# Kernel tuning notes

Measured on AMD Instinct MI355X. Metric: run time of the kernel, lower is better.

## Reference

```python
import jax, jax.numpy as jnp
import numpy as np

WAY = 5  # N_way from init


def setup_inputs() -> dict:
    key = jax.random.key(0)
    k1, k2, k3, k4 = jax.random.split(key, 4)
    N, c, h, w = 80, 2048, 16, 16
    S = 512  # shuffle_num
    x = jax.random.normal(k1, (N, c, h, w), dtype=jnp.float32)
    s_ca = jax.random.uniform(k2, (N, c, 1, 1), dtype=jnp.float32)
    # random channel indices per sample (stand-in for random.sample)
    rand_index = jax.random.randint(k3, (N, S), 0, c)
    # partner offset per sample (stand-in for random j != i)
    partner = jax.random.randint(k4, (N,), 0, N - 1)
    return {"x": x, "s_ca": s_ca, "rand_index": rand_index,
            "partner": partner, "shuffle_num": S}


def reference(x, s_ca, rand_index, partner, shuffle_num):
    N, c, h, w = x.shape
    way = WAY
    scores = s_ca.reshape(N, c)
    # per-sample top-k channels by attention score
    _, topk_idx = jax.lax.top_k(scores, shuffle_num)          # [N, S]
    # partner sample j != i (offset trick guarantees inequality)
    j = (jnp.arange(N) + 1 + partner) % N                      # [N]
    bi = jnp.arange(N)[:, None]                                # [N, 1]
    x_topk = x[bi, topk_idx]                                   # [N, S, h, w]
    x_part = x[j[:, None], rand_index]                         # [N, S, h, w]
    blend = 0.7 * x_topk + 0.3 * x_part
    # scatter blended channels back (batched gather-blend-scatter)
    aug_x = x.at[bi, topk_idx].set(blend)                      # [N, c, h, w]
    # group into (way, shot, ...) and concat original + augmented episodes
    x_r = x.reshape(way, -1, c, h, w)
    aug_r = aug_x.reshape(way, -1, c, h, w)
    out = jnp.concatenate((x_r, aug_r), axis=1)                # [way, 2*shot, c, h, w]
    s = s_ca.reshape(way, -1, c, 1, 1)
    s = jnp.concatenate((s, s), axis=1)                        # repeat(1,2,1,1,1)
    out = out * s
    return out.reshape(-1, c, h, w)                            # [2N, c, h, w]
```

## Files before the change

kernel.cpp:

```cpp
#include <hip/hip_runtime.h>

#define N_SAMP 80
#define C_CH   2048
#define HW     256
#define S_TOP  512
#define HW4    64

__global__ __launch_bounds__(256) void rank_lds_kernel(
    const float* __restrict__ s_ca, int* __restrict__ rank) {
  __shared__ unsigned long long keys[C_CH];
  const int n = blockIdx.x >> 3;
  const int tid = threadIdx.x;
  const float* __restrict__ row = s_ca + (size_t)n * C_CH;

  for (int i = tid; i < C_CH; i += 256) {
    unsigned int b = __float_as_uint(row[i]);
    b ^= (b & 0x80000000u) ? 0xFFFFFFFFu : 0x80000000u;
    keys[i] = ((unsigned long long)b << 11) |
              (unsigned long long)(C_CH - 1 - i);
  }
  __syncthreads();

  const int i = ((blockIdx.x & 7) << 8) | tid;
  const unsigned long long ki = keys[i];
  int cnt = 0;
#pragma unroll 16
  for (int j = 0; j < C_CH; ++j) {
    cnt += (keys[j] > ki) ? 1 : 0;
  }
  rank[(size_t)n * C_CH + i] = (cnt < S_TOP) ? cnt : -1;
}

__global__ __launch_bounds__(256) void shuffle_out_fused(
    const float4* __restrict__ x4, const float* __restrict__ s_ca,
    const int* __restrict__ rand_index, const int* __restrict__ partner,
    const int* __restrict__ rank, float4* __restrict__ out4) {
  const unsigned int lane = threadIdx.x & 63u;
  const unsigned int pw = blockIdx.x * 4u + (threadIdx.x >> 6);
  const unsigned int n = pw >> 11;
  const unsigned int ch = pw & 2047u;
  const unsigned int g = n >> 4;
  const unsigned int b = n & 15u;

  const size_t out_plain =
      (((size_t)((g << 5) | b) * C_CH + ch) << 6) | lane;
  const size_t out_aug = out_plain + ((size_t)(16 * C_CH) << 6);

  const float s = s_ca[pw];
  const float4 v = x4[((size_t)pw << 6) | lane];
  float4 pv = make_float4(v.x * s, v.y * s, v.z * s, v.w * s);
  float4 av = pv;

  const int k = rank[pw];
  if (k >= 0) {
    int jn = (int)n + 1 + partner[n];
    if (jn >= N_SAMP) jn -= N_SAMP;
    const int pc = rand_index[(size_t)n * S_TOP + k];
    const float4 u = x4[((((size_t)jn << 11) | (size_t)pc) << 6) | lane];
    av.x = (0.7f * v.x + 0.3f * u.x) * s;
    av.y = (0.7f * v.y + 0.3f * u.y) * s;
    av.z = (0.7f * v.z + 0.3f * u.z) * s;
    av.w = (0.7f * v.w + 0.3f * u.w) * s;
  }

  out4[out_plain] = pv;
  out4[out_aug] = av;
}

extern "C" void kernel_launch(void* const* d_in, const int* in_sizes, int n_in,
                              void* d_out, int out_size, void* d_ws,
                              size_t ws_size, hipStream_t stream) {
  const float* x = (const float*)d_in[0];
  const float* s_ca = (const float*)d_in[1];
  const int* rand_index = (const int*)d_in[2];
  const int* partner = (const int*)d_in[3];

  int* rank = (int*)d_ws;

  rank_lds_kernel<<<N_SAMP * 8, 256, 0, stream>>>(s_ca, rank);

  const int nblocks = (N_SAMP * C_CH) / 4;
  shuffle_out_fused<<<nblocks, 256, 0, stream>>>(
      (const float4*)x, s_ca, rand_index, partner, rank, (float4*)d_out);
}
```

Measured before the change: 478.1 us.

## Fuse top-k rank computation into shuffle kernel via wavefront ballot counting

Removes the separate LDS-based rank kernel and its workspace round trip. Each wavefront now computes its channel's rank directly inside the output kernel by scanning the 2048 scores of its sample row with float4 loads, ballot and popcount, breaking ties by index. This saves a kernel launch and the rank buffer traffic. In exchange every wavefront rereads an 8 KB score row and does 32 ballots, which adds redundant compute and cache traffic to a kernel that is otherwise bandwidth bound.

Result: faster. 459.1 us (-4.0%).

```diff
diff --git a/kernel.cpp b/kernel.cpp
--- a/kernel.cpp
+++ b/kernel.cpp
@@ -6,35 +6,10 @@
 #define S_TOP  512
 #define HW4    64
 
-__global__ __launch_bounds__(256) void rank_lds_kernel(
-    const float* __restrict__ s_ca, int* __restrict__ rank) {
-  __shared__ unsigned long long keys[C_CH];
-  const int n = blockIdx.x >> 3;
-  const int tid = threadIdx.x;
-  const float* __restrict__ row = s_ca + (size_t)n * C_CH;
-
-  for (int i = tid; i < C_CH; i += 256) {
-    unsigned int b = __float_as_uint(row[i]);
-    b ^= (b & 0x80000000u) ? 0xFFFFFFFFu : 0x80000000u;
-    keys[i] = ((unsigned long long)b << 11) |
-              (unsigned long long)(C_CH - 1 - i);
-  }
-  __syncthreads();
-
-  const int i = ((blockIdx.x & 7) << 8) | tid;
-  const unsigned long long ki = keys[i];
-  int cnt = 0;
-#pragma unroll 16
-  for (int j = 0; j < C_CH; ++j) {
-    cnt += (keys[j] > ki) ? 1 : 0;
-  }
-  rank[(size_t)n * C_CH + i] = (cnt < S_TOP) ? cnt : -1;
-}
-
-__global__ __launch_bounds__(256) void shuffle_out_fused(
+__global__ __launch_bounds__(256) void fused_shuffle_kernel(
     const float4* __restrict__ x4, const float* __restrict__ s_ca,
     const int* __restrict__ rand_index, const int* __restrict__ partner,
-    const int* __restrict__ rank, float4* __restrict__ out4) {
+    float4* __restrict__ out4) {
   const unsigned int lane = threadIdx.x & 63u;
   const unsigned int pw = blockIdx.x * 4u + (threadIdx.x >> 6);
   const unsigned int n = pw >> 11;
@@ -46,21 +21,35 @@
       (((size_t)((g << 5) | b) * C_CH + ch) << 6) | lane;
   const size_t out_aug = out_plain + ((size_t)(16 * C_CH) << 6);
 
-  const float s = s_ca[pw];
+  const float* __restrict__ row = s_ca + (size_t)n * C_CH;
+  const float si = row[ch];
+
   const float4 v = x4[((size_t)pw << 6) | lane];
-  float4 pv = make_float4(v.x * s, v.y * s, v.z * s, v.w * s);
+
+  const float4* __restrict__ row4 = (const float4*)row;
+  int cnt = 0;
+#pragma unroll
+  for (int q = 0; q < 8; ++q) {
+    const float4 sv = row4[q * 64 + lane];
+    const unsigned int j0 = 4u * (q * 64u + lane);
+    cnt += __popcll(__ballot(sv.x > si || (sv.x == si && (j0 + 0u) < ch)));
+    cnt += __popcll(__ballot(sv.y > si || (sv.y == si && (j0 + 1u) < ch)));
+    cnt += __popcll(__ballot(sv.z > si || (sv.z == si && (j0 + 2u) < ch)));
+    cnt += __popcll(__ballot(sv.w > si || (sv.w == si && (j0 + 3u) < ch)));
+  }
+
+  float4 pv = make_float4(v.x * si, v.y * si, v.z * si, v.w * si);
   float4 av = pv;
 
-  const int k = rank[pw];
-  if (k >= 0) {
+  if (cnt < S_TOP) {
     int jn = (int)n + 1 + partner[n];
     if (jn >= N_SAMP) jn -= N_SAMP;
-    const int pc = rand_index[(size_t)n * S_TOP + k];
+    const int pc = rand_index[(size_t)n * S_TOP + cnt];
     const float4 u = x4[((((size_t)jn << 11) | (size_t)pc) << 6) | lane];
-    av.x = (0.7f * v.x + 0.3f * u.x) * s;
-    av.y = (0.7f * v.y + 0.3f * u.y) * s;
-    av.z = (0.7f * v.z + 0.3f * u.z) * s;
-    av.w = (0.7f * v.w + 0.3f * u.w) * s;
+    av.x = (0.7f * v.x + 0.3f * u.x) * si;
+    av.y = (0.7f * v.y + 0.3f * u.y) * si;
+    av.z = (0.7f * v.z + 0.3f * u.z) * si;
+    av.w = (0.7f * v.w + 0.3f * u.w) * si;
   }
 
   out4[out_plain] = pv;
@@ -75,11 +64,7 @@
   const int* rand_index = (const int*)d_in[2];
   const int* partner = (const int*)d_in[3];
 
-  int* rank = (int*)d_ws;
-
-  rank_lds_kernel<<<N_SAMP * 8, 256, 0, stream>>>(s_ca, rank);
-
   const int nblocks = (N_SAMP * C_CH) / 4;
-  shuffle_out_fused<<<nblocks, 256, 0, stream>>>(
-      (const float4*)x, s_ca, rand_index, partner, rank, (float4*)d_out);
+  fused_shuffle_kernel<<<nblocks, 256, 0, stream>>>(
+      (const float4*)x, s_ca, rand_index, partner, (float4*)d_out);
 }
```
